# Kernel tuning notes

Hardware: AMD Instinct MI355X
Metric: run time of the kernel (lower is better)

The kernel has to match this reference:

```python
import jax, jax.numpy as jnp
import numpy as np

B, N, H, V = 8192, 12, 512, 256  # batch, n_columns, hidden_size, per-column vocab
LN_EPS = 1e-5


def setup_inputs() -> dict:
    key = jax.random.key(0)
    k0, k1, k2, k3 = jax.random.split(key, 4)
    return {
        "input_embedding": jax.random.normal(k0, (B, H), dtype=jnp.float32),
        "features": jax.random.randint(k1, (B, N), 0, V),  # one categorical id per column
        "emb_tables": jax.random.normal(k2, (N, V, H), dtype=jnp.float32) * 0.02,
        "ln_gamma": jnp.ones((2 * H,), dtype=jnp.float32),
        "ln_beta": jnp.zeros((2 * H,), dtype=jnp.float32),
        "pred_W": jax.random.normal(k3, (N, 2 * H, V), dtype=jnp.float32) * 0.02,
        "pred_b": jnp.zeros((N, V), dtype=jnp.float32),
    }


def reference(input_embedding, features, emb_tables, ln_gamma, ln_beta, pred_W, pred_b):
    n = features.shape[1]
    # per-column embedding lookup: emb[b, n] = emb_tables[n, features[b, n]]  -> [B, N, H]
    emb = emb_tables[jnp.arange(n)[None, :], features]
    # _make_masked_sums: triu(diagonal=1) mask summed over dim 1 == exclusive prefix sum
    # over the column axis: masked_sums[b, j] = sum_{i < j} emb[b, i]
    masked_sums = jnp.cumsum(emb, axis=1) - emb  # [B, N, H]
    ctx = jnp.broadcast_to(input_embedding[:, None, :], emb.shape)  # [B, N, H]
    x = jnp.concatenate([ctx, masked_sums], axis=-1)  # [B, N, 2H]
    # LayerNorm over last dim, then exact (erf) GELU as in torch nn.GELU default
    mu = jnp.mean(x, axis=-1, keepdims=True)
    var = jnp.mean(jnp.square(x - mu), axis=-1, keepdims=True)
    xn = (x - mu) * jax.lax.rsqrt(var + LN_EPS) * ln_gamma + ln_beta
    act = jax.nn.gelu(xn, approximate=False)
    # per-column predictor heads: logits[b, n, :] = act[b, n, :] @ pred_W[n] + pred_b[n]
    logits = jnp.einsum('bnh,nhv->bnv', act, pred_W) + pred_b
    return logits
```

## Files before the change

### kernel.cpp

```cpp
#include <hip/hip_runtime.h>
#include <stdint.h>

#define B_SZ 8192
#define N_F 12
#define H_DIM 512
#define K_DIM 1024
#define V_DIM 256

typedef __attribute__((ext_vector_type(8))) __bf16 bf16x8;
typedef __attribute__((ext_vector_type(4))) float f32x4;

__device__ inline float gelu_f(float x) {
  float t = 1.5957691216057308f * x * (1.0f + 0.044715f * x * x);
  return x / (1.0f + __expf(-t));
}

__device__ inline void gld_lds16(const void* g, void* l) {
  __builtin_amdgcn_global_load_lds(
      (const __attribute__((address_space(1))) void*)g,
      (__attribute__((address_space(3))) void*)l, 16, 0, 0);
}

__global__ __launch_bounds__(256, 8) void k_prep(
    const float* __restrict__ ie, const int* __restrict__ feat,
    const float* __restrict__ tab, const float* __restrict__ gam,
    const float* __restrict__ bet, __bf16* __restrict__ act2,
    float* __restrict__ stats) {
  const int lane = threadIdx.x & 63;
  const int b = blockIdx.x * 4 + (threadIdx.x >> 6);

  const float* cb = ie + (size_t)b * H_DIM + lane * 8;
  float4 c0 = *(const float4*)cb;
  float4 c1 = *(const float4*)(cb + 4);
  float s = c0.x + c0.y + c0.z + c0.w + c1.x + c1.y + c1.z + c1.w;
  float q = c0.x * c0.x + c0.y * c0.y + c0.z * c0.z + c0.w * c0.w +
            c1.x * c1.x + c1.y * c1.y + c1.z * c1.z + c1.w * c1.w;
#pragma unroll
  for (int o = 1; o < 64; o <<= 1) {
    s += __shfl_xor(s, o, 64);
    q += __shfl_xor(q, o, 64);
  }
  const float S1 = s, Q1 = q;

  const float4 g0 = *(const float4*)(gam + H_DIM + lane * 8);
  const float4 g1 = *(const float4*)(gam + H_DIM + lane * 8 + 4);
  const float4 e0 = *(const float4*)(bet + H_DIM + lane * 8);
  const float4 e1 = *(const float4*)(bet + H_DIM + lane * 8 + 4);

  float r[8];
#pragma unroll
  for (int i = 0; i < 8; ++i) r[i] = 0.f;

  const int sw = (lane & ~7) | ((lane & 7) ^ (b & 7));
  __bf16* arow = act2 + (size_t)b * H_DIM + sw * 8;

  for (int n = 0; n < N_F; ++n) {
    s = 0.f; q = 0.f;
#pragma unroll
    for (int i = 0; i < 8; ++i) { s += r[i]; q += r[i] * r[i]; }
#pragma unroll
    for (int o = 1; o < 64; o <<= 1) {
      s += __shfl_xor(s, o, 64);
      q += __shfl_xor(q, o, 64);
    }
    const float mean = (S1 + s) * (1.0f / 1024.0f);
    const float var = (Q1 + q) * (1.0f / 1024.0f) - mean * mean;
    const float rs = rsqrtf(var + 1e-5f);
    if (lane == 0)
      *(float2*)(stats + ((size_t)b * N_F + n) * 2) = make_float2(mean, rs);

    bf16x8 pk;
    pk[0] = (__bf16)gelu_f((r[0] - mean) * rs * g0.x + e0.x);
    pk[1] = (__bf16)gelu_f((r[1] - mean) * rs * g0.y + e0.y);
    pk[2] = (__bf16)gelu_f((r[2] - mean) * rs * g0.z + e0.z);
    pk[3] = (__bf16)gelu_f((r[3] - mean) * rs * g0.w + e0.w);
    pk[4] = (__bf16)gelu_f((r[4] - mean) * rs * g1.x + e1.x);
    pk[5] = (__bf16)gelu_f((r[5] - mean) * rs * g1.y + e1.y);
    pk[6] = (__bf16)gelu_f((r[6] - mean) * rs * g1.z + e1.z);
    pk[7] = (__bf16)gelu_f((r[7] - mean) * rs * g1.w + e1.w);
    *(bf16x8*)(arow + (size_t)n * B_SZ * H_DIM) = pk;

    if (n < N_F - 1) {
      const int f = feat[b * N_F + n];
      const float* tr = tab + ((size_t)n * V_DIM + f) * H_DIM + lane * 8;
      const float4 t0 = *(const float4*)tr;
      const float4 t1 = *(const float4*)(tr + 4);
      r[0] += t0.x; r[1] += t0.y; r[2] += t0.z; r[3] += t0.w;
      r[4] += t1.x; r[5] += t1.y; r[6] += t1.z; r[7] += t1.w;
    }
  }
}

__global__ __launch_bounds__(256) void k_wt(const float* __restrict__ W,
                                            __bf16* __restrict__ Wt) {
  __shared__ float tile[32][33];
  const int bid = blockIdx.x;
  const int n = bid >> 8;
  const int rem = bid & 255;
  const int kt = rem >> 3, vt = rem & 7;
  const int tx = threadIdx.x & 31, ty = threadIdx.x >> 5;
  const float* src = W + (size_t)n * K_DIM * V_DIM;
#pragma unroll
  for (int i = 0; i < 4; ++i) {
    const int k = kt * 32 + ty + i * 8;
    tile[ty + i * 8][tx] = src[(size_t)k * V_DIM + vt * 32 + tx];
  }
  __syncthreads();
  __bf16* dst = Wt + (size_t)n * V_DIM * K_DIM;
  const int t = threadIdx.x;
  if (t < 128) {
    const int v_l = t >> 2, c_l = t & 3;
    const int v = vt * 32 + v_l;
    bf16x8 pk;
#pragma unroll
    for (int e = 0; e < 8; ++e) pk[e] = (__bf16)tile[c_l * 8 + e][v_l];
    const int gc = kt * 4 + c_l;
    const int swc = (gc & ~7) | ((gc & 7) ^ (v & 7));
    *(bf16x8*)(dst + (size_t)v * K_DIM + swc * 8) = pk;
  }
}

__global__ __launch_bounds__(512, 4) void k_gemm(
    const float* __restrict__ ie, const __bf16* __restrict__ act2,
    const __bf16* __restrict__ Wt, const float* __restrict__ stats,
    const float* __restrict__ gam, const float* __restrict__ bet,
    const float* __restrict__ bias, float* __restrict__ out) {
  constexpr int BM = 128, BN = 256, BK = 64;
  __shared__ __align__(16) __bf16 As[BM * BK];
  __shared__ __align__(16) __bf16 Ws[BN * BK];
  __shared__ float muL[BM], rsL[BM];

  const int n = blockIdx.y;
  const int b0 = blockIdx.x * BM;
  const int t = threadIdx.x;
  const int lane = t & 63;
  const int w = t >> 6;
  const int wm = w & 1;
  const int wn = w >> 1;
  const int l15 = lane & 15;
  const int lq = lane >> 4;

  if (t < 2 * BM) {
    const int r = t >> 1, which = t & 1;
    const float v = stats[((size_t)(b0 + r) * N_F + n) * 2 + which];
    if (which == 0) muL[r] = v; else rsL[r] = v;
  }

  f32x4 acc[4][4];
#pragma unroll
  for (int i = 0; i < 4; ++i)
#pragma unroll
    for (int j = 0; j < 4; ++j) acc[i][j] = (f32x4){0.f, 0.f, 0.f, 0.f};

  const __bf16* act2n = act2 + (size_t)n * B_SZ * H_DIM;
  const __bf16* Wtn = Wt + (size_t)n * V_DIM * K_DIM;

  const int o8 = t & 7;
  const int rA = t >> 3;
  const int lr8 = lane >> 3;
  const int lo8 = lane & 7;

  for (int kt = 0; kt < 16; ++kt) {
    const int k0 = kt * BK;
    __syncthreads();
#pragma unroll
    for (int p = 0; p < 4; ++p) {
      const int v0 = w * 32 + p * 8;
      gld_lds16(Wtn + (size_t)(v0 + lr8) * K_DIM + k0 + lo8 * 8, Ws + v0 * BK);
    }
    if (k0 < H_DIM) {
      const int kk = k0 + o8 * 8;
      const float4 gg0 = *(const float4*)(gam + kk);
      const float4 gg1 = *(const float4*)(gam + kk + 4);
      const float4 bt0 = *(const float4*)(bet + kk);
      const float4 bt1 = *(const float4*)(bet + kk + 4);
      const int swo = (o8 ^ (rA & 7)) * 8;
#pragma unroll
      for (int half = 0; half < 2; ++half) {
        const int r = rA + half * 64;
        const float* cp = ie + (size_t)(b0 + r) * H_DIM + kk;
        const float4 x0 = *(const float4*)cp;
        const float4 x1 = *(const float4*)(cp + 4);
        const float mu = muL[r], rs = rsL[r];
        bf16x8 pk;
        pk[0] = (__bf16)gelu_f((x0.x - mu) * rs * gg0.x + bt0.x);
        pk[1] = (__bf16)gelu_f((x0.y - mu) * rs * gg0.y + bt0.y);
        pk[2] = (__bf16)gelu_f((x0.z - mu) * rs * gg0.z + bt0.z);
        pk[3] = (__bf16)gelu_f((x0.w - mu) * rs * gg0.w + bt0.w);
        pk[4] = (__bf16)gelu_f((x1.x - mu) * rs * gg1.x + bt1.x);
        pk[5] = (__bf16)gelu_f((x1.y - mu) * rs * gg1.y + bt1.y);
        pk[6] = (__bf16)gelu_f((x1.z - mu) * rs * gg1.z + bt1.z);
        pk[7] = (__bf16)gelu_f((x1.w - mu) * rs * gg1.w + bt1.w);
        *(bf16x8*)(As + r * BK + swo) = pk;
      }
    } else {
#pragma unroll
      for (int p = 0; p < 2; ++p) {
        const int r0 = w * 16 + p * 8;
        gld_lds16(act2n + (size_t)(b0 + r0 + lr8) * H_DIM + (k0 - H_DIM) + lo8 * 8,
                  As + r0 * BK);
      }
    }
    __syncthreads();
#pragma unroll
    for (int ks = 0; ks < 2; ++ks) {
      const int cs = ks * 4 + lq;
      bf16x8 af[4], bb[4];
#pragma unroll
      for (int i = 0; i < 4; ++i) {
        const int row = wm * 64 + i * 16 + l15;
        af[i] = *(const bf16x8*)(As + row * BK + ((cs ^ (row & 7)) << 3));
      }
#pragma unroll
      for (int j = 0; j < 4; ++j) {
        const int row = wn * 64 + j * 16 + l15;
        bb[j] = *(const bf16x8*)(Ws + row * BK + ((cs ^ (row & 7)) << 3));
      }
#pragma unroll
      for (int i = 0; i < 4; ++i)
#pragma unroll
        for (int j = 0; j < 4; ++j)
          acc[i][j] =
              __builtin_amdgcn_mfma_f32_16x16x32_bf16(af[i], bb[j], acc[i][j], 0, 0, 0);
    }
  }

#pragma unroll
  for (int j = 0; j < 4; ++j) {
    const int v = wn * 64 + j * 16 + l15;
    const float bv = bias[n * V_DIM + v];
#pragma unroll
    for (int i = 0; i < 4; ++i) {
      const int rb = wm * 64 + i * 16 + lq * 4;
#pragma unroll
      for (int r = 0; r < 4; ++r) {
        out[((size_t)(b0 + rb + r) * N_F + n) * V_DIM + v] = acc[i][j][r] + bv;
      }
    }
  }
}

extern "C" void kernel_launch(void* const* d_in, const int* in_sizes, int n_in,
                              void* d_out, int out_size, void* d_ws, size_t ws_size,
                              hipStream_t stream) {
  const float* ie = (const float*)d_in[0];
  const int* feat = (const int*)d_in[1];
  const float* tab = (const float*)d_in[2];
  const float* gam = (const float*)d_in[3];
  const float* bet = (const float*)d_in[4];
  const float* predW = (const float*)d_in[5];
  const float* predb = (const float*)d_in[6];
  float* out = (float*)d_out;

  char* ws = (char*)d_ws;
  __bf16* act2 = (__bf16*)ws;
  float* stats = (float*)(ws + 100663296);
  __bf16* Wt = (__bf16*)(ws + 100663296 + 786432);

  hipLaunchKernelGGL(k_prep, dim3(B_SZ / 4), dim3(256), 0, stream, ie, feat,
                     tab, gam, bet, act2, stats);
  hipLaunchKernelGGL(k_wt, dim3(3072), dim3(256), 0, stream, predW, Wt);
  hipLaunchKernelGGL(k_gemm, dim3(B_SZ / 128, N_F), dim3(512), 0, stream, ie,
                     act2, Wt, stats, gam, bet, predb, out);
}
```

Before: 279.4 us.

## Batch LN stat reductions in prep kernel and stage GEMM epilogue through LDS

The prep kernel now loads all feature ids and table rows up front, computes per-column sums in one pass, and does a single batched shuffle reduction for all twelve columns instead of a serial reduce per column. The launch-bounds occupancy hint drops from 8 to 4 to make room for the extra registers. The GEMM epilogue writes accumulators into a shared-memory tile that reuses the A/W buffers, then stores full rows as coalesced float4 writes instead of scattered scalar stores. This costs extra barriers and a second round of table loads in prep.

```diff
diff --git a/kernel.cpp b/kernel.cpp
--- a/kernel.cpp
+++ b/kernel.cpp
@@ -21,7 +21,7 @@
       (__attribute__((address_space(3))) void*)l, 16, 0, 0);
 }
 
-__global__ __launch_bounds__(256, 8) void k_prep(
+__global__ __launch_bounds__(256, 4) void k_prep(
     const float* __restrict__ ie, const int* __restrict__ feat,
     const float* __restrict__ tab, const float* __restrict__ gam,
     const float* __restrict__ bet, __bf16* __restrict__ act2,
@@ -30,59 +30,85 @@
   const int b = blockIdx.x * 4 + (threadIdx.x >> 6);
 
   const float* cb = ie + (size_t)b * H_DIM + lane * 8;
-  float4 c0 = *(const float4*)cb;
-  float4 c1 = *(const float4*)(cb + 4);
-  float s = c0.x + c0.y + c0.z + c0.w + c1.x + c1.y + c1.z + c1.w;
-  float q = c0.x * c0.x + c0.y * c0.y + c0.z * c0.z + c0.w * c0.w +
-            c1.x * c1.x + c1.y * c1.y + c1.z * c1.z + c1.w * c1.w;
+  const float4 c0 = *(const float4*)cb;
+  const float4 c1 = *(const float4*)(cb + 4);
+  float sc = c0.x + c0.y + c0.z + c0.w + c1.x + c1.y + c1.z + c1.w;
+  float qc = c0.x * c0.x + c0.y * c0.y + c0.z * c0.z + c0.w * c0.w +
+             c1.x * c1.x + c1.y * c1.y + c1.z * c1.z + c1.w * c1.w;
+
+  int f[N_F - 1];
+  const int* fr = feat + b * N_F;
+#pragma unroll
+  for (int n = 0; n < N_F - 1; ++n) f[n] = fr[n];
+
+  float r[8];
+#pragma unroll
+  for (int i = 0; i < 8; ++i) r[i] = 0.f;
+  float snl[N_F], qnl[N_F];
+#pragma unroll
+  for (int n = 0; n < N_F; ++n) {
+    float s = 0.f, q = 0.f;
+#pragma unroll
+    for (int i = 0; i < 8; ++i) { s += r[i]; q += r[i] * r[i]; }
+    snl[n] = s;
+    qnl[n] = q;
+    if (n < N_F - 1) {
+      const float* tr = tab + ((size_t)n * V_DIM + f[n]) * H_DIM + lane * 8;
+      const float4 t0 = *(const float4*)tr;
+      const float4 t1 = *(const float4*)(tr + 4);
+      r[0] += t0.x; r[1] += t0.y; r[2] += t0.z; r[3] += t0.w;
+      r[4] += t1.x; r[5] += t1.y; r[6] += t1.z; r[7] += t1.w;
+    }
+  }
+
 #pragma unroll
   for (int o = 1; o < 64; o <<= 1) {
-    s += __shfl_xor(s, o, 64);
-    q += __shfl_xor(q, o, 64);
-  }
-  const float S1 = s, Q1 = q;
+    sc += __shfl_xor(sc, o, 64);
+    qc += __shfl_xor(qc, o, 64);
+#pragma unroll
+    for (int n = 0; n < N_F; ++n) {
+      snl[n] += __shfl_xor(snl[n], o, 64);
+      qnl[n] += __shfl_xor(qnl[n], o, 64);
+    }
+  }
+
+  float mean[N_F], rsg[N_F];
+#pragma unroll
+  for (int n = 0; n < N_F; ++n) {
+    const float m = (sc + snl[n]) * (1.0f / 1024.0f);
+    const float var = (qc + qnl[n]) * (1.0f / 1024.0f) - m * m;
+    mean[n] = m;
+    rsg[n] = rsqrtf(var + 1e-5f);
+  }
+  if (lane == 0) {
+    float* sp = stats + (size_t)b * N_F * 2;
+#pragma unroll
+    for (int n = 0; n < N_F; ++n)
+      *(float2*)(sp + n * 2) = make_float2(mean[n], rsg[n]);
+  }
 
   const float4 g0 = *(const float4*)(gam + H_DIM + lane * 8);
   const float4 g1 = *(const float4*)(gam + H_DIM + lane * 8 + 4);
   const float4 e0 = *(const float4*)(bet + H_DIM + lane * 8);
   const float4 e1 = *(const float4*)(bet + H_DIM + lane * 8 + 4);
-
-  float r[8];
+  const float ga[8] = {g0.x, g0.y, g0.z, g0.w, g1.x, g1.y, g1.z, g1.w};
+  const float be[8] = {e0.x, e0.y, e0.z, e0.w, e1.x, e1.y, e1.z, e1.w};
+
 #pragma unroll
   for (int i = 0; i < 8; ++i) r[i] = 0.f;
-
   const int sw = (lane & ~7) | ((lane & 7) ^ (b & 7));
   __bf16* arow = act2 + (size_t)b * H_DIM + sw * 8;
 
+#pragma unroll
   for (int n = 0; n < N_F; ++n) {
-    s = 0.f; q = 0.f;
-#pragma unroll
-    for (int i = 0; i < 8; ++i) { s += r[i]; q += r[i] * r[i]; }
-#pragma unroll
-    for (int o = 1; o < 64; o <<= 1) {
-      s += __shfl_xor(s, o, 64);
-      q += __shfl_xor(q, o, 64);
-    }
-    const float mean = (S1 + s) * (1.0f / 1024.0f);
-    const float var = (Q1 + q) * (1.0f / 1024.0f) - mean * mean;
-    const float rs = rsqrtf(var + 1e-5f);
-    if (lane == 0)
-      *(float2*)(stats + ((size_t)b * N_F + n) * 2) = make_float2(mean, rs);
-
+    const float m = mean[n], rs = rsg[n];
     bf16x8 pk;
-    pk[0] = (__bf16)gelu_f((r[0] - mean) * rs * g0.x + e0.x);
-    pk[1] = (__bf16)gelu_f((r[1] - mean) * rs * g0.y + e0.y);
-    pk[2] = (__bf16)gelu_f((r[2] - mean) * rs * g0.z + e0.z);
-    pk[3] = (__bf16)gelu_f((r[3] - mean) * rs * g0.w + e0.w);
-    pk[4] = (__bf16)gelu_f((r[4] - mean) * rs * g1.x + e1.x);
-    pk[5] = (__bf16)gelu_f((r[5] - mean) * rs * g1.y + e1.y);
-    pk[6] = (__bf16)gelu_f((r[6] - mean) * rs * g1.z + e1.z);
-    pk[7] = (__bf16)gelu_f((r[7] - mean) * rs * g1.w + e1.w);
+#pragma unroll
+    for (int i = 0; i < 8; ++i)
+      pk[i] = (__bf16)gelu_f((r[i] - m) * rs * ga[i] + be[i]);
     *(bf16x8*)(arow + (size_t)n * B_SZ * H_DIM) = pk;
-
     if (n < N_F - 1) {
-      const int f = feat[b * N_F + n];
-      const float* tr = tab + ((size_t)n * V_DIM + f) * H_DIM + lane * 8;
+      const float* tr = tab + ((size_t)n * V_DIM + f[n]) * H_DIM + lane * 8;
       const float4 t0 = *(const float4*)tr;
       const float4 t1 = *(const float4*)(tr + 4);
       r[0] += t0.x; r[1] += t0.y; r[2] += t0.z; r[3] += t0.w;
@@ -126,8 +152,10 @@
     const float* __restrict__ gam, const float* __restrict__ bet,
     const float* __restrict__ bias, float* __restrict__ out) {
   constexpr int BM = 128, BN = 256, BK = 64;
-  __shared__ __align__(16) __bf16 As[BM * BK];
-  __shared__ __align__(16) __bf16 Ws[BN * BK];
+  __shared__ __align__(16) char smem[49152];
+  __bf16* As = (__bf16*)smem;
+  __bf16* Ws = (__bf16*)(smem + BM * BK * 2);
+  float* ldsf = (float*)smem;
   __shared__ float muL[BM], rsL[BM];
 
   const int n = blockIdx.y;
@@ -225,17 +253,30 @@
     }
   }
 
-#pragma unroll
-  for (int j = 0; j < 4; ++j) {
-    const int v = wn * 64 + j * 16 + l15;
-    const float bv = bias[n * V_DIM + v];
-#pragma unroll
-    for (int i = 0; i < 4; ++i) {
-      const int rb = wm * 64 + i * 16 + lq * 4;
-#pragma unroll
-      for (int r = 0; r < 4; ++r) {
-        out[((size_t)(b0 + rb + r) * N_F + n) * V_DIM + v] = acc[i][j][r] + bv;
-      }
+  float bv[4];
+#pragma unroll
+  for (int j = 0; j < 4; ++j) bv[j] = bias[n * V_DIM + wn * 64 + j * 16 + l15];
+
+  const int erow = t >> 4;
+  const int ecol0 = (t & 15) * 4;
+#pragma unroll
+  for (int i = 0; i < 4; ++i) {
+    __syncthreads();
+#pragma unroll
+    for (int j = 0; j < 4; ++j) {
+      const int col = wn * 64 + j * 16 + l15;
+      const int lr = wm * 16 + lq * 4;
+#pragma unroll
+      for (int r = 0; r < 4; ++r)
+        ldsf[(lr + r) * 260 + col] = acc[i][j][r] + bv[j];
+    }
+    __syncthreads();
+    const int grow = b0 + (erow < 16 ? (i * 16 + erow) : (64 + i * 16 + erow - 16));
+    float* orow = out + ((size_t)grow * N_F + n) * V_DIM;
+#pragma unroll
+    for (int c = 0; c < 4; ++c) {
+      const int col = ecol0 + c * 64;
+      *(float4*)(orow + col) = *(const float4*)(ldsf + erow * 260 + col);
     }
   }
 }
```

Measured after the change: 330.4 us. +18.3%, slower.

## Materialize full LN+GELU activation in prep kernel instead of recomputing in GEMM

Applied to the files above, without the earlier changes.

The prep kernel now computes LayerNorm+GELU for both the context half and the masked-sum half and writes a full 1024-wide bf16 activation per (column, row). The GEMM drops its per-tile GELU computation and stats loading and loads every A tile with async global-to-LDS copies. This simplifies the GEMM main loop and removes transcendental work there, but it doubles the activation buffer written and read through HBM. Prep launch bounds are loosened to allow more registers.

```diff
diff --git a/kernel.cpp b/kernel.cpp
--- a/kernel.cpp
+++ b/kernel.cpp
@@ -21,41 +21,48 @@
       (__attribute__((address_space(3))) void*)l, 16, 0, 0);
 }
 
-__global__ __launch_bounds__(256, 8) void k_prep(
+__global__ __launch_bounds__(256, 4) void k_prep(
     const float* __restrict__ ie, const int* __restrict__ feat,
     const float* __restrict__ tab, const float* __restrict__ gam,
-    const float* __restrict__ bet, __bf16* __restrict__ act2,
-    float* __restrict__ stats) {
+    const float* __restrict__ bet, __bf16* __restrict__ act) {
   const int lane = threadIdx.x & 63;
   const int b = blockIdx.x * 4 + (threadIdx.x >> 6);
 
   const float* cb = ie + (size_t)b * H_DIM + lane * 8;
-  float4 c0 = *(const float4*)cb;
-  float4 c1 = *(const float4*)(cb + 4);
-  float s = c0.x + c0.y + c0.z + c0.w + c1.x + c1.y + c1.z + c1.w;
-  float q = c0.x * c0.x + c0.y * c0.y + c0.z * c0.z + c0.w * c0.w +
-            c1.x * c1.x + c1.y * c1.y + c1.z * c1.z + c1.w * c1.w;
+  const float4 c0 = *(const float4*)cb;
+  const float4 c1 = *(const float4*)(cb + 4);
+  const float c[8] = {c0.x, c0.y, c0.z, c0.w, c1.x, c1.y, c1.z, c1.w};
+  float sc = c[0] + c[1] + c[2] + c[3] + c[4] + c[5] + c[6] + c[7];
+  float qc = c[0] * c[0] + c[1] * c[1] + c[2] * c[2] + c[3] * c[3] +
+             c[4] * c[4] + c[5] * c[5] + c[6] * c[6] + c[7] * c[7];
 #pragma unroll
   for (int o = 1; o < 64; o <<= 1) {
-    s += __shfl_xor(s, o, 64);
-    q += __shfl_xor(q, o, 64);
-  }
-  const float S1 = s, Q1 = q;
-
-  const float4 g0 = *(const float4*)(gam + H_DIM + lane * 8);
-  const float4 g1 = *(const float4*)(gam + H_DIM + lane * 8 + 4);
-  const float4 e0 = *(const float4*)(bet + H_DIM + lane * 8);
-  const float4 e1 = *(const float4*)(bet + H_DIM + lane * 8 + 4);
+    sc += __shfl_xor(sc, o, 64);
+    qc += __shfl_xor(qc, o, 64);
+  }
+
+  const float4 ga0 = *(const float4*)(gam + lane * 8);
+  const float4 ga1 = *(const float4*)(gam + lane * 8 + 4);
+  const float4 eb0 = *(const float4*)(bet + lane * 8);
+  const float4 eb1 = *(const float4*)(bet + lane * 8 + 4);
+  const float g1[8] = {ga0.x, ga0.y, ga0.z, ga0.w, ga1.x, ga1.y, ga1.z, ga1.w};
+  const float b1[8] = {eb0.x, eb0.y, eb0.z, eb0.w, eb1.x, eb1.y, eb1.z, eb1.w};
+  const float4 gb0 = *(const float4*)(gam + H_DIM + lane * 8);
+  const float4 gb1 = *(const float4*)(gam + H_DIM + lane * 8 + 4);
+  const float4 fb0 = *(const float4*)(bet + H_DIM + lane * 8);
+  const float4 fb1 = *(const float4*)(bet + H_DIM + lane * 8 + 4);
+  const float g2[8] = {gb0.x, gb0.y, gb0.z, gb0.w, gb1.x, gb1.y, gb1.z, gb1.w};
+  const float b2[8] = {fb0.x, fb0.y, fb0.z, fb0.w, fb1.x, fb1.y, fb1.z, fb1.w};
 
   float r[8];
 #pragma unroll
   for (int i = 0; i < 8; ++i) r[i] = 0.f;
 
   const int sw = (lane & ~7) | ((lane & 7) ^ (b & 7));
-  __bf16* arow = act2 + (size_t)b * H_DIM + sw * 8;
+  const int fbase = b * N_F;
 
   for (int n = 0; n < N_F; ++n) {
-    s = 0.f; q = 0.f;
+    float s = 0.f, q = 0.f;
 #pragma unroll
     for (int i = 0; i < 8; ++i) { s += r[i]; q += r[i] * r[i]; }
 #pragma unroll
@@ -63,25 +70,23 @@
       s += __shfl_xor(s, o, 64);
       q += __shfl_xor(q, o, 64);
     }
-    const float mean = (S1 + s) * (1.0f / 1024.0f);
-    const float var = (Q1 + q) * (1.0f / 1024.0f) - mean * mean;
+    const float mean = (sc + s) * (1.0f / 1024.0f);
+    const float var = (qc + q) * (1.0f / 1024.0f) - mean * mean;
     const float rs = rsqrtf(var + 1e-5f);
-    if (lane == 0)
-      *(float2*)(stats + ((size_t)b * N_F + n) * 2) = make_float2(mean, rs);
-
-    bf16x8 pk;
-    pk[0] = (__bf16)gelu_f((r[0] - mean) * rs * g0.x + e0.x);
-    pk[1] = (__bf16)gelu_f((r[1] - mean) * rs * g0.y + e0.y);
-    pk[2] = (__bf16)gelu_f((r[2] - mean) * rs * g0.z + e0.z);
-    pk[3] = (__bf16)gelu_f((r[3] - mean) * rs * g0.w + e0.w);
-    pk[4] = (__bf16)gelu_f((r[4] - mean) * rs * g1.x + e1.x);
-    pk[5] = (__bf16)gelu_f((r[5] - mean) * rs * g1.y + e1.y);
-    pk[6] = (__bf16)gelu_f((r[6] - mean) * rs * g1.z + e1.z);
-    pk[7] = (__bf16)gelu_f((r[7] - mean) * rs * g1.w + e1.w);
-    *(bf16x8*)(arow + (size_t)n * B_SZ * H_DIM) = pk;
+
+    __bf16* arow = act + ((size_t)n * B_SZ + b) * K_DIM;
+    bf16x8 p1, p2;
+#pragma unroll
+    for (int i = 0; i < 8; ++i)
+      p1[i] = (__bf16)gelu_f((c[i] - mean) * rs * g1[i] + b1[i]);
+#pragma unroll
+    for (int i = 0; i < 8; ++i)
+      p2[i] = (__bf16)gelu_f((r[i] - mean) * rs * g2[i] + b2[i]);
+    *(bf16x8*)(arow + sw * 8) = p1;
+    *(bf16x8*)(arow + H_DIM + sw * 8) = p2;
 
     if (n < N_F - 1) {
-      const int f = feat[b * N_F + n];
+      const int f = feat[fbase + n];
       const float* tr = tab + ((size_t)n * V_DIM + f) * H_DIM + lane * 8;
       const float4 t0 = *(const float4*)tr;
       const float4 t1 = *(const float4*)(tr + 4);
@@ -121,14 +126,11 @@
 }
 
 __global__ __launch_bounds__(512, 4) void k_gemm(
-    const float* __restrict__ ie, const __bf16* __restrict__ act2,
-    const __bf16* __restrict__ Wt, const float* __restrict__ stats,
-    const float* __restrict__ gam, const float* __restrict__ bet,
+    const __bf16* __restrict__ act, const __bf16* __restrict__ Wt,
     const float* __restrict__ bias, float* __restrict__ out) {
   constexpr int BM = 128, BN = 256, BK = 64;
   __shared__ __align__(16) __bf16 As[BM * BK];
   __shared__ __align__(16) __bf16 Ws[BN * BK];
-  __shared__ float muL[BM], rsL[BM];
 
   const int n = blockIdx.y;
   const int b0 = blockIdx.x * BM;
@@ -140,23 +142,15 @@
   const int l15 = lane & 15;
   const int lq = lane >> 4;
 
-  if (t < 2 * BM) {
-    const int r = t >> 1, which = t & 1;
-    const float v = stats[((size_t)(b0 + r) * N_F + n) * 2 + which];
-    if (which == 0) muL[r] = v; else rsL[r] = v;
-  }
-
   f32x4 acc[4][4];
 #pragma unroll
   for (int i = 0; i < 4; ++i)
 #pragma unroll
     for (int j = 0; j < 4; ++j) acc[i][j] = (f32x4){0.f, 0.f, 0.f, 0.f};
 
-  const __bf16* act2n = act2 + (size_t)n * B_SZ * H_DIM;
+  const __bf16* actn = act + ((size_t)n * B_SZ + b0) * K_DIM;
   const __bf16* Wtn = Wt + (size_t)n * V_DIM * K_DIM;
 
-  const int o8 = t & 7;
-  const int rA = t >> 3;
   const int lr8 = lane >> 3;
   const int lo8 = lane & 7;
 
@@ -168,38 +162,10 @@
       const int v0 = w * 32 + p * 8;
       gld_lds16(Wtn + (size_t)(v0 + lr8) * K_DIM + k0 + lo8 * 8, Ws + v0 * BK);
     }
-    if (k0 < H_DIM) {
-      const int kk = k0 + o8 * 8;
-      const float4 gg0 = *(const float4*)(gam + kk);
-      const float4 gg1 = *(const float4*)(gam + kk + 4);
-      const float4 bt0 = *(const float4*)(bet + kk);
-      const float4 bt1 = *(const float4*)(bet + kk + 4);
-      const int swo = (o8 ^ (rA & 7)) * 8;
-#pragma unroll
-      for (int half = 0; half < 2; ++half) {
-        const int r = rA + half * 64;
-        const float* cp = ie + (size_t)(b0 + r) * H_DIM + kk;
-        const float4 x0 = *(const float4*)cp;
-        const float4 x1 = *(const float4*)(cp + 4);
-        const float mu = muL[r], rs = rsL[r];
-        bf16x8 pk;
-        pk[0] = (__bf16)gelu_f((x0.x - mu) * rs * gg0.x + bt0.x);
-        pk[1] = (__bf16)gelu_f((x0.y - mu) * rs * gg0.y + bt0.y);
-        pk[2] = (__bf16)gelu_f((x0.z - mu) * rs * gg0.z + bt0.z);
-        pk[3] = (__bf16)gelu_f((x0.w - mu) * rs * gg0.w + bt0.w);
-        pk[4] = (__bf16)gelu_f((x1.x - mu) * rs * gg1.x + bt1.x);
-        pk[5] = (__bf16)gelu_f((x1.y - mu) * rs * gg1.y + bt1.y);
-        pk[6] = (__bf16)gelu_f((x1.z - mu) * rs * gg1.z + bt1.z);
-        pk[7] = (__bf16)gelu_f((x1.w - mu) * rs * gg1.w + bt1.w);
-        *(bf16x8*)(As + r * BK + swo) = pk;
-      }
-    } else {
-#pragma unroll
-      for (int p = 0; p < 2; ++p) {
-        const int r0 = w * 16 + p * 8;
-        gld_lds16(act2n + (size_t)(b0 + r0 + lr8) * H_DIM + (k0 - H_DIM) + lo8 * 8,
-                  As + r0 * BK);
-      }
+#pragma unroll
+    for (int p = 0; p < 2; ++p) {
+      const int r0 = w * 16 + p * 8;
+      gld_lds16(actn + (size_t)(r0 + lr8) * K_DIM + k0 + lo8 * 8, As + r0 * BK);
     }
     __syncthreads();
 #pragma unroll
@@ -253,13 +219,12 @@
   float* out = (float*)d_out;
 
   char* ws = (char*)d_ws;
-  __bf16* act2 = (__bf16*)ws;
-  float* stats = (float*)(ws + 100663296);
-  __bf16* Wt = (__bf16*)(ws + 100663296 + 786432);
+  __bf16* act = (__bf16*)ws;
+  __bf16* Wt = (__bf16*)(ws + 201326592);
 
   hipLaunchKernelGGL(k_prep, dim3(B_SZ / 4), dim3(256), 0, stream, ie, feat,
-                     tab, gam, bet, act2, stats);
+                     tab, gam, bet, act);
   hipLaunchKernelGGL(k_wt, dim3(3072), dim3(256), 0, stream, predW, Wt);
-  hipLaunchKernelGGL(k_gemm, dim3(B_SZ / 128, N_F), dim3(512), 0, stream, ie,
-                     act2, Wt, stats, gam, bet, predb, out);
-}
+  hipLaunchKernelGGL(k_gemm, dim3(B_SZ / 128, N_F), dim3(512), 0, stream, act,
+                     Wt, predb, out);
+}
```

Measured after the change: 292.0 us. 1.05x slower.
